# Performance work log

Measured on AMD Instinct MI355X. Metric: run time of the kernel, lower is better.

The kernel has to match this reference:

```python
import jax, jax.numpy as jnp
import numpy as np

B, S, D, UNITS = 8, 2048, 512, 512

def setup_inputs() -> dict:
    key = jax.random.key(0)
    k1, k2, k3, k4, k5 = jax.random.split(key, 5)
    inputs = jax.random.normal(k1, (B, S, D), dtype=jnp.float32)
    scale = 1.0 / np.sqrt(D)
    Ww = jax.random.normal(k2, (D, UNITS), dtype=jnp.float32) * scale
    Wb = jnp.zeros((UNITS,), dtype=jnp.float32)
    Uw = jax.random.normal(k3, (D, UNITS), dtype=jnp.float32) * scale
    Ub = jnp.zeros((UNITS,), dtype=jnp.float32)
    return {"inputs": inputs, "Ww": Ww, "Wb": Wb, "Uw": Uw, "Ub": Ub}

def reference(inputs, Ww, Wb, Uw, Ub):
    # query/key projections: [B,S,units]
    query = jnp.einsum('bsd,du->bsu', inputs, Ww) + Wb
    key_ = jnp.einsum('bsd,du->bsu', inputs, Uw) + Ub
    # unscaled scores [B,S,S], softmax over last axis
    scores = jnp.einsum('bqu,bku->bqk', query, key_)
    attn = jax.nn.softmax(scores, axis=-1)
    # context uses raw inputs as values
    context = jnp.einsum('bqk,bkd->bqd', attn, inputs)
    return context
```

## Files before the change

kernel.cpp:

```cpp
#include <hip/hip_runtime.h>
#include <stdint.h>

#define B_ 8
#define S_ 2048
#define D_ 512
#define U_ 512
#define M_TOTAL (B_*S_)
#define NPROJ (2*U_)

typedef __attribute__((ext_vector_type(8))) _Float16 f16x8;
typedef __attribute__((ext_vector_type(4))) float f32x4;

__device__ __forceinline__ uint16_t f2h(float f){
  return __builtin_bit_cast(uint16_t, (_Float16)f);
}

__device__ __forceinline__ void gload16(const void* g, void* l){
  __builtin_amdgcn_global_load_lds(
      (const __attribute__((address_space(1))) void*)g,
      (__attribute__((address_space(3))) void*)l, 16, 0, 0);
}

template<int ROWS>
__device__ __forceinline__ void stage_half(char* lbase, const uint16_t* __restrict__ gpanel,
                                           int ld, int wv, int lane){
  int r0 = wv*8 + (lane>>3);
  int gs = ((lane&7) ^ (r0&7)) << 3;
  gload16(gpanel + (size_t)r0*ld + gs, lbase + wv*1024);
  if constexpr (ROWS==128){
    gload16(gpanel + (size_t)(r0+64)*ld + gs, lbase + 8192 + wv*1024);
  }
}

__global__ __launch_bounds__(256) void prep_w(const float* __restrict__ Ww,
                                              const float* __restrict__ Uw,
                                              uint16_t* __restrict__ WT){
  int idx = blockIdx.x*256 + threadIdx.x;
  int u = idx >> 9;
  int d = idx & 511;
  float v = (u < U_) ? Ww[d*U_ + u] : Uw[d*U_ + (u-U_)];
  WT[idx] = f2h(v);
}

__global__ __launch_bounds__(256) void prep_x(const float* __restrict__ X,
                                              uint16_t* __restrict__ Xf,
                                              uint16_t* __restrict__ XT){
  __shared__ float tile[32][33];
  int b = blockIdx.z;
  int s0 = blockIdx.x * 32;
  int d0 = blockIdx.y * 32;
  int tid = threadIdx.x;
  int tr = tid >> 5;
  int tc = tid & 31;
  const float* Xb = X + (size_t)b*S_*D_;
#pragma unroll
  for (int i = 0; i < 32; i += 8){
    size_t off = (size_t)(s0+tr+i)*D_ + d0+tc;
    float v = Xb[off];
    tile[tr+i][tc] = v;
    Xf[(size_t)b*S_*D_ + off] = f2h(v);
  }
  __syncthreads();
  uint16_t* XTb = XT + (size_t)b*D_*S_;
#pragma unroll
  for (int i = 0; i < 32; i += 8)
    XTb[(size_t)(d0+tr+i)*S_ + s0+tc] = f2h(tile[tc][tr+i]);
}

#define MODE_PROJ 0
#define MODE_SCORES 1
#define MODE_PV 2

template<int MODE, int BM>
__global__ __launch_bounds__(512, 2) void gemm8p(
    const uint16_t* __restrict__ A, long long strideA, int lda,
    const uint16_t* __restrict__ Bp, long long strideB, int ldb,
    float* __restrict__ Cf, long long strideC, int ldc,
    uint16_t* __restrict__ Qo, uint16_t* __restrict__ Ko,
    const float* __restrict__ biasW, const float* __restrict__ biasU,
    int KD)
{
  constexpr int BMH   = BM/2;
  constexpr int MFR   = BMH/16;
  constexpr int AHALF = BMH*128;
  constexpr int BHALF = 128*128;
  constexpr int DSTR  = 2*AHALF + 2*BHALF;
  constexpr int ALOADS = (BMH==128) ? 2 : 1;
  __shared__ __align__(16) char smem[2*DSTR];

  const int z  = blockIdx.z;
  const int m0 = blockIdx.y * BM;
  const int n0 = blockIdx.x * 256;
  const uint16_t* Apan = A  + strideA*z + (size_t)m0*lda;
  const uint16_t* Bpan = Bp + strideB*z + (size_t)n0*ldb;

  const int t512 = threadIdx.x;
  const int wv   = t512 >> 6;
  const int lane = t512 & 63;
  const int wm   = wv >> 2;
  const int wn   = wv & 3;
  const int fr   = lane & 15;
  const int fg   = lane >> 4;
  const int sw   = fr & 7;

  const int NT = KD >> 6;

  auto Aslot = [&](int par, int h){ return smem + par*DSTR + h*AHALF; };
  auto Bslot = [&](int par, int h){ return smem + par*DSTR + 2*AHALF + h*BHALF; };

  stage_half<BMH>(Aslot(0,0), Apan,                      lda, wv, lane);
  stage_half<BMH>(Aslot(0,1), Apan + (size_t)BMH*lda,    lda, wv, lane);
  stage_half<128>(Bslot(0,0), Bpan,                      ldb, wv, lane);
  stage_half<128>(Bslot(0,1), Bpan + (size_t)128*ldb,    ldb, wv, lane);
  if (NT > 1)
    stage_half<BMH>(Aslot(1,0), Apan + 64,               lda, wv, lane);
  if constexpr (ALOADS==2) asm volatile("s_waitcnt vmcnt(2)" ::: "memory");
  else                     asm volatile("s_waitcnt vmcnt(1)" ::: "memory");
  __builtin_amdgcn_s_barrier();

  f32x4 acc[MFR][4];
#pragma unroll
  for (int i=0;i<MFR;i++)
#pragma unroll
    for (int j=0;j<4;j++) acc[i][j] = (f32x4){0.f,0.f,0.f,0.f};

  for (int t = 0; t < NT; ++t){
    const int p = t & 1;
    const char* myA = Aslot(p, wm);
    const char* myB = Bslot(p, wn>>1);
    f16x8 af[MFR];

    auto rdA = [&](int ks){
#pragma unroll
      for (int mf=0; mf<MFR; ++mf)
        af[mf] = *(const f16x8*)(myA + (mf*16+fr)*128 + (((ks<<2)|fg) ^ sw)*16);
    };
    auto rdB = [&](int ks, int nh, f16x8& b0, f16x8& b1){
      int rb = (wn&1)*64 + nh*32 + fr;
      b0 = *(const f16x8*)(myB + rb*128      + (((ks<<2)|fg) ^ sw)*16);
      b1 = *(const f16x8*)(myB + (rb+16)*128 + (((ks<<2)|fg) ^ sw)*16);
    };
    auto mm = [&](int nh, f16x8 b0, f16x8 b1){
      __builtin_amdgcn_s_setprio(1);
#pragma unroll
      for (int mf=0; mf<MFR; ++mf){
        acc[mf][nh*2]   = __builtin_amdgcn_mfma_f32_16x16x32_f16(af[mf], b0, acc[mf][nh*2],   0,0,0);
        acc[mf][nh*2+1] = __builtin_amdgcn_mfma_f32_16x16x32_f16(af[mf], b1, acc[mf][nh*2+1], 0,0,0);
      }
      __builtin_amdgcn_s_setprio(0);
    };

    f16x8 b0, b1;
    rdA(0); rdB(0, 0, b0, b1);
    if (t+1 < NT)
      stage_half<BMH>(Aslot(p^1,1), Apan + (size_t)BMH*lda + (t+1)*64, lda, wv, lane);
    __builtin_amdgcn_s_barrier();
    mm(0, b0, b1);
    __builtin_amdgcn_s_barrier();
    rdB(0, 1, b0, b1);
    if (t+1 < NT)
      stage_half<128>(Bslot(p^1,0), Bpan + (t+1)*64, ldb, wv, lane);
    __builtin_amdgcn_s_barrier();
    mm(1, b0, b1);
    __builtin_amdgcn_s_barrier();
    rdA(1); rdB(1, 0, b0, b1);
    if (t+1 < NT)
      stage_half<128>(Bslot(p^1,1), Bpan + (size_t)128*ldb + (t+1)*64, ldb, wv, lane);
    __builtin_amdgcn_s_barrier();
    mm(0, b0, b1);
    __builtin_amdgcn_s_barrier();
    rdB(1, 1, b0, b1);
    if (t+2 < NT)
      stage_half<BMH>(Aslot(p,0), Apan + (t+2)*64, lda, wv, lane);
    __builtin_amdgcn_s_barrier();
    mm(1, b0, b1);
    if constexpr (ALOADS==2) asm volatile("s_waitcnt vmcnt(2)" ::: "memory");
    else                     asm volatile("s_waitcnt vmcnt(1)" ::: "memory");
    __builtin_amdgcn_s_barrier();
  }

#pragma unroll
  for (int mf=0; mf<MFR; ++mf)
#pragma unroll
    for (int nf=0; nf<4; ++nf){
      int col  = n0 + wn*64 + nf*16 + fr;
      int rowb = m0 + wm*BMH + mf*16 + fg*4;
      f32x4 a = acc[mf][nf];
      if constexpr (MODE==MODE_PROJ){
        float bias = (col < U_) ? biasW[col] : biasU[col - U_];
        if (col < U_){
#pragma unroll
          for (int r=0;r<4;r++) Qo[(size_t)(rowb+r)*U_ + col] = f2h(a[r] + bias);
        } else {
#pragma unroll
          for (int r=0;r<4;r++) Ko[(size_t)(rowb+r)*U_ + col - U_] = f2h(a[r] + bias);
        }
      } else {
        float* C = Cf + strideC*z;
#pragma unroll
        for (int r=0;r<4;r++)
          C[(size_t)(rowb+r)*ldc + col] = a[r];
      }
    }
}

__global__ __launch_bounds__(256) void softmax_rows(float* __restrict__ SPbase)
{
  const long long row = (long long)blockIdx.y * S_ + blockIdx.x;
  float* Srow = SPbase + row * (long long)S_;
  const int t = threadIdx.x;
  const int lane = t & 63, wave = t >> 6;
  float4 x0 = *((const float4*)Srow + t*2);
  float4 x1 = *((const float4*)Srow + t*2 + 1);
  float v[8] = {x0.x,x0.y,x0.z,x0.w,x1.x,x1.y,x1.z,x1.w};
  float mx = v[0];
#pragma unroll
  for (int j=1;j<8;j++) mx = fmaxf(mx, v[j]);
#pragma unroll
  for (int off=1; off<64; off<<=1) mx = fmaxf(mx, __shfl_xor(mx, off));
  __shared__ float redm[4], reds[4];
  if (lane==0) redm[wave] = mx;
  __syncthreads();
  mx = fmaxf(fmaxf(redm[0],redm[1]), fmaxf(redm[2],redm[3]));
  float sum = 0.f;
#pragma unroll
  for (int j=0;j<8;j++){ v[j] = expf(v[j]-mx); sum += v[j]; }
#pragma unroll
  for (int off=1; off<64; off<<=1) sum += __shfl_xor(sum, off);
  if (lane==0) reds[wave] = sum;
  __syncthreads();
  sum = reds[0]+reds[1]+reds[2]+reds[3];
  float inv = 1.0f / sum;
  uint16_t o[8];
#pragma unroll
  for (int j=0;j<8;j++) o[j] = f2h(v[j]*inv);
  uint16_t* Prow = (uint16_t*)Srow;
  *((ushort4*)Prow + t*2)     = make_ushort4(o[0],o[1],o[2],o[3]);
  *((ushort4*)Prow + t*2 + 1) = make_ushort4(o[4],o[5],o[6],o[7]);
}

extern "C" void kernel_launch(void* const* d_in, const int* in_sizes, int n_in,
                              void* d_out, int out_size, void* d_ws, size_t ws_size,
                              hipStream_t stream)
{
  (void)in_sizes; (void)n_in; (void)out_size;
  const float* X  = (const float*)d_in[0];
  const float* Ww = (const float*)d_in[1];
  const float* Wb = (const float*)d_in[2];
  const float* Uw = (const float*)d_in[3];
  const float* Ub = (const float*)d_in[4];
  float* out = (float*)d_out;

  char* ws = (char*)d_ws;
  size_t off = 0;
  uint16_t* Xf = (uint16_t*)(ws + off); off += (size_t)M_TOTAL*D_*2;
  uint16_t* XT = (uint16_t*)(ws + off); off += (size_t)B_*D_*S_*2;
  uint16_t* WT = (uint16_t*)(ws + off); off += (size_t)NPROJ*D_*2;
  uint16_t* Qf = (uint16_t*)(ws + off); off += (size_t)M_TOTAL*U_*2;
  uint16_t* Kf = (uint16_t*)(ws + off); off += (size_t)M_TOTAL*U_*2;
  char* SP = ws + off;
  size_t per_b = (size_t)S_*S_*4;
  int g = 8;
  while (g > 1 && off + per_b*(size_t)g > ws_size) g >>= 1;

  prep_w<<<dim3((NPROJ*D_)/256), 256, 0, stream>>>(Ww, Uw, WT);
  prep_x<<<dim3(S_/32, D_/32, B_), 256, 0, stream>>>(X, Xf, XT);

  gemm8p<MODE_PROJ,256><<<dim3(NPROJ/256, M_TOTAL/256, 1), 512, 0, stream>>>(
      Xf, 0, D_, WT, 0, D_,
      nullptr, 0, 0, Qf, Kf, Wb, Ub, D_);

  for (int b0 = 0; b0 < B_; b0 += g) {
    gemm8p<MODE_SCORES,256><<<dim3(S_/256, S_/256, g), 512, 0, stream>>>(
        Qf + (size_t)b0*S_*U_, (long long)S_*U_, U_,
        Kf + (size_t)b0*S_*U_, (long long)S_*U_, U_,
        (float*)SP, (long long)S_*S_, S_,
        nullptr, nullptr, nullptr, nullptr, U_);
    softmax_rows<<<dim3(S_, g), 256, 0, stream>>>((float*)SP);
    gemm8p<MODE_PV,128><<<dim3(D_/256, S_/128, g), 512, 0, stream>>>(
        (const uint16_t*)SP, 2LL*S_*S_, 2*S_,
        XT + (size_t)b0*D_*S_, (long long)D_*S_, S_,
        out + (size_t)b0*S_*D_, (long long)S_*D_, D_,
        nullptr, nullptr, nullptr, nullptr, S_);
  }
}
```

Before: 163.6 us.

## Fuse scores, softmax and PV into a single flash-attention kernel

Replaces the separate scores GEMM, row softmax and PV GEMM with one flash-attention kernel that streams K and V tiles through LDS and keeps an online max and sum per query row. This removes the materialized fp32 SxS score matrix and its write and reread traffic. The kernel also skips rescaling the accumulator unless the running max grows by more than a threshold. It uses small 64x64 tiles with many barriers per iteration, and the K staging is only partly overlapped with compute, so MFMA utilization may be lower than in the tuned GEMM.

```diff
diff --git a/kernel.cpp b/kernel.cpp
--- a/kernel.cpp
+++ b/kernel.cpp
@@ -7,6 +7,9 @@
 #define U_ 512
 #define M_TOTAL (B_*S_)
 #define NPROJ (2*U_)
+#define QBLK 64
+#define KVBLK 64
+#define NIT (S_/KVBLK)
 
 typedef __attribute__((ext_vector_type(8))) _Float16 f16x8;
 typedef __attribute__((ext_vector_type(4))) float f32x4;
@@ -67,32 +70,24 @@
     XTb[(size_t)(d0+tr+i)*S_ + s0+tc] = f2h(tile[tc][tr+i]);
 }
 
-#define MODE_PROJ 0
-#define MODE_SCORES 1
-#define MODE_PV 2
-
-template<int MODE, int BM>
-__global__ __launch_bounds__(512, 2) void gemm8p(
-    const uint16_t* __restrict__ A, long long strideA, int lda,
-    const uint16_t* __restrict__ Bp, long long strideB, int ldb,
-    float* __restrict__ Cf, long long strideC, int ldc,
+__global__ __launch_bounds__(512, 2) void gemm_proj(
+    const uint16_t* __restrict__ A, int lda,
+    const uint16_t* __restrict__ Bp, int ldb,
     uint16_t* __restrict__ Qo, uint16_t* __restrict__ Ko,
     const float* __restrict__ biasW, const float* __restrict__ biasU,
     int KD)
 {
-  constexpr int BMH   = BM/2;
-  constexpr int MFR   = BMH/16;
+  constexpr int BMH   = 128;
+  constexpr int MFR   = 8;
   constexpr int AHALF = BMH*128;
   constexpr int BHALF = 128*128;
   constexpr int DSTR  = 2*AHALF + 2*BHALF;
-  constexpr int ALOADS = (BMH==128) ? 2 : 1;
   __shared__ __align__(16) char smem[2*DSTR];
 
-  const int z  = blockIdx.z;
-  const int m0 = blockIdx.y * BM;
+  const int m0 = blockIdx.y * 256;
   const int n0 = blockIdx.x * 256;
-  const uint16_t* Apan = A  + strideA*z + (size_t)m0*lda;
-  const uint16_t* Bpan = Bp + strideB*z + (size_t)n0*ldb;
+  const uint16_t* Apan = A  + (size_t)m0*lda;
+  const uint16_t* Bpan = Bp + (size_t)n0*ldb;
 
   const int t512 = threadIdx.x;
   const int wv   = t512 >> 6;
@@ -108,14 +103,13 @@
   auto Aslot = [&](int par, int h){ return smem + par*DSTR + h*AHALF; };
   auto Bslot = [&](int par, int h){ return smem + par*DSTR + 2*AHALF + h*BHALF; };
 
-  stage_half<BMH>(Aslot(0,0), Apan,                      lda, wv, lane);
-  stage_half<BMH>(Aslot(0,1), Apan + (size_t)BMH*lda,    lda, wv, lane);
-  stage_half<128>(Bslot(0,0), Bpan,                      ldb, wv, lane);
-  stage_half<128>(Bslot(0,1), Bpan + (size_t)128*ldb,    ldb, wv, lane);
+  stage_half<128>(Aslot(0,0), Apan,                   lda, wv, lane);
+  stage_half<128>(Aslot(0,1), Apan + (size_t)128*lda, lda, wv, lane);
+  stage_half<128>(Bslot(0,0), Bpan,                   ldb, wv, lane);
+  stage_half<128>(Bslot(0,1), Bpan + (size_t)128*ldb, ldb, wv, lane);
   if (NT > 1)
-    stage_half<BMH>(Aslot(1,0), Apan + 64,               lda, wv, lane);
-  if constexpr (ALOADS==2) asm volatile("s_waitcnt vmcnt(2)" ::: "memory");
-  else                     asm volatile("s_waitcnt vmcnt(1)" ::: "memory");
+    stage_half<128>(Aslot(1,0), Apan + 64,            lda, wv, lane);
+  asm volatile("s_waitcnt vmcnt(2)" ::: "memory");
   __builtin_amdgcn_s_barrier();
 
   f32x4 acc[MFR][4];
@@ -153,7 +147,7 @@
     f16x8 b0, b1;
     rdA(0); rdB(0, 0, b0, b1);
     if (t+1 < NT)
-      stage_half<BMH>(Aslot(p^1,1), Apan + (size_t)BMH*lda + (t+1)*64, lda, wv, lane);
+      stage_half<128>(Aslot(p^1,1), Apan + (size_t)128*lda + (t+1)*64, lda, wv, lane);
     __builtin_amdgcn_s_barrier();
     mm(0, b0, b1);
     __builtin_amdgcn_s_barrier();
@@ -171,11 +165,10 @@
     __builtin_amdgcn_s_barrier();
     rdB(1, 1, b0, b1);
     if (t+2 < NT)
-      stage_half<BMH>(Aslot(p,0), Apan + (t+2)*64, lda, wv, lane);
+      stage_half<128>(Aslot(p,0), Apan + (t+2)*64, lda, wv, lane);
     __builtin_amdgcn_s_barrier();
     mm(1, b0, b1);
-    if constexpr (ALOADS==2) asm volatile("s_waitcnt vmcnt(2)" ::: "memory");
-    else                     asm volatile("s_waitcnt vmcnt(1)" ::: "memory");
+    asm volatile("s_waitcnt vmcnt(2)" ::: "memory");
     __builtin_amdgcn_s_barrier();
   }
 
@@ -184,66 +177,208 @@
 #pragma unroll
     for (int nf=0; nf<4; ++nf){
       int col  = n0 + wn*64 + nf*16 + fr;
-      int rowb = m0 + wm*BMH + mf*16 + fg*4;
+      int rowb = m0 + wm*128 + mf*16 + fg*4;
       f32x4 a = acc[mf][nf];
-      if constexpr (MODE==MODE_PROJ){
-        float bias = (col < U_) ? biasW[col] : biasU[col - U_];
-        if (col < U_){
-#pragma unroll
-          for (int r=0;r<4;r++) Qo[(size_t)(rowb+r)*U_ + col] = f2h(a[r] + bias);
-        } else {
-#pragma unroll
-          for (int r=0;r<4;r++) Ko[(size_t)(rowb+r)*U_ + col - U_] = f2h(a[r] + bias);
-        }
+      float bias = (col < U_) ? biasW[col] : biasU[col - U_];
+      if (col < U_){
+#pragma unroll
+        for (int r=0;r<4;r++) Qo[(size_t)(rowb+r)*U_ + col] = f2h(a[r] + bias);
       } else {
-        float* C = Cf + strideC*z;
-#pragma unroll
-        for (int r=0;r<4;r++)
-          C[(size_t)(rowb+r)*ldc + col] = a[r];
+#pragma unroll
+        for (int r=0;r<4;r++) Ko[(size_t)(rowb+r)*U_ + col - U_] = f2h(a[r] + bias);
       }
     }
 }
 
-__global__ __launch_bounds__(256) void softmax_rows(float* __restrict__ SPbase)
+__global__ __launch_bounds__(512, 2) void flash_attn(
+    const uint16_t* __restrict__ Qf,
+    const uint16_t* __restrict__ Kf,
+    const uint16_t* __restrict__ XT,
+    float* __restrict__ Out)
 {
-  const long long row = (long long)blockIdx.y * S_ + blockIdx.x;
-  float* Srow = SPbase + row * (long long)S_;
-  const int t = threadIdx.x;
-  const int lane = t & 63, wave = t >> 6;
-  float4 x0 = *((const float4*)Srow + t*2);
-  float4 x1 = *((const float4*)Srow + t*2 + 1);
-  float v[8] = {x0.x,x0.y,x0.z,x0.w,x1.x,x1.y,x1.z,x1.w};
-  float mx = v[0];
-#pragma unroll
-  for (int j=1;j<8;j++) mx = fmaxf(mx, v[j]);
-#pragma unroll
-  for (int off=1; off<64; off<<=1) mx = fmaxf(mx, __shfl_xor(mx, off));
-  __shared__ float redm[4], reds[4];
-  if (lane==0) redm[wave] = mx;
-  __syncthreads();
-  mx = fmaxf(fmaxf(redm[0],redm[1]), fmaxf(redm[2],redm[3]));
-  float sum = 0.f;
-#pragma unroll
-  for (int j=0;j<8;j++){ v[j] = expf(v[j]-mx); sum += v[j]; }
-#pragma unroll
-  for (int off=1; off<64; off<<=1) sum += __shfl_xor(sum, off);
-  if (lane==0) reds[wave] = sum;
-  __syncthreads();
-  sum = reds[0]+reds[1]+reds[2]+reds[3];
-  float inv = 1.0f / sum;
-  uint16_t o[8];
-#pragma unroll
-  for (int j=0;j<8;j++) o[j] = f2h(v[j]*inv);
-  uint16_t* Prow = (uint16_t*)Srow;
-  *((ushort4*)Prow + t*2)     = make_ushort4(o[0],o[1],o[2],o[3]);
-  *((ushort4*)Prow + t*2 + 1) = make_ushort4(o[4],o[5],o[6],o[7]);
+  __shared__ __align__(16) uint16_t Ks[KVBLK][512];
+  __shared__ __align__(16) uint16_t Vs[512][KVBLK];
+  __shared__ __align__(16) float    Ss[QBLK][68];
+  __shared__ __align__(16) uint16_t Ps[QBLK][KVBLK];
+  __shared__ float m_s[QBLK], l_s[QBLK], f_s[QBLK];
+
+  const int bid   = blockIdx.x;
+  const int batch = bid & 7;
+  const int mblk  = bid >> 3;
+  const int s0    = mblk * QBLK;
+
+  const int t    = threadIdx.x;
+  const int wv   = t >> 6;
+  const int lane = t & 63;
+  const int fr   = lane & 15;
+  const int fg   = lane >> 4;
+  const int qg = wv >> 1;
+  const int kh = wv & 1;
+  const int wm = wv >> 2;
+  const int wd = wv & 3;
+
+  const uint16_t* Qrow = Qf + ((size_t)batch*S_ + s0)*U_;
+  const uint16_t* Krow = Kf + (size_t)batch*S_*U_;
+  const uint16_t* Vt   = XT + (size_t)batch*D_*S_;
+
+  f16x8 qreg[16];
+#pragma unroll
+  for (int kk=0; kk<16; ++kk)
+    qreg[kk] = *(const f16x8*)(Qrow + (size_t)(qg*16+fr)*U_ + kk*32 + fg*8);
+
+  auto stageK = [&](int ti){
+    const uint16_t* src = Krow + (size_t)(ti*KVBLK)*U_;
+#pragma unroll
+    for (int i=0;i<8;++i){
+      int r = i*8 + wv;
+      gload16(src + (size_t)r*U_ + ((lane ^ (r&7))<<3),
+              (char*)Ks + i*8192 + wv*1024);
+    }
+  };
+  auto stageV = [&](int ti){
+    const uint16_t* src = Vt + ti*KVBLK;
+#pragma unroll
+    for (int i=0;i<8;++i){
+      int d = i*64 + wv*8 + (lane>>3);
+      int g = lane & 7;
+      gload16(src + (size_t)d*S_ + ((g ^ (d&7))<<3),
+              (char*)Vs + i*8192 + wv*1024);
+    }
+  };
+
+  stageK(0);
+  if (t < QBLK){ m_s[t] = -3e38f; l_s[t] = 0.f; }
+  f32x4 acc[2][8];
+#pragma unroll
+  for (int i=0;i<2;i++)
+#pragma unroll
+    for (int j=0;j<8;j++) acc[i][j] = (f32x4){0.f,0.f,0.f,0.f};
+  asm volatile("s_waitcnt lgkmcnt(0)" ::: "memory");
+  __builtin_amdgcn_s_barrier();
+
+  for (int it=0; it<NIT; ++it){
+    stageV(it);
+    asm volatile("s_waitcnt vmcnt(8)" ::: "memory");
+
+    f32x4 sfr0 = (f32x4){0.f,0.f,0.f,0.f};
+    f32x4 sfr1 = (f32x4){0.f,0.f,0.f,0.f};
+    __builtin_amdgcn_s_setprio(1);
+#pragma unroll
+    for (int kk=0; kk<16; ++kk){
+      int gA = kk*4 + fg;
+      int kr0 = kh*32 + fr;
+      int kr1 = kh*32 + 16 + fr;
+      f16x8 bv0 = *(const f16x8*)((const char*)Ks + kr0*1024 + ((gA ^ (kr0&7))<<4));
+      f16x8 bv1 = *(const f16x8*)((const char*)Ks + kr1*1024 + ((gA ^ (kr1&7))<<4));
+      sfr0 = __builtin_amdgcn_mfma_f32_16x16x32_f16(qreg[kk], bv0, sfr0, 0,0,0);
+      sfr1 = __builtin_amdgcn_mfma_f32_16x16x32_f16(qreg[kk], bv1, sfr1, 0,0,0);
+    }
+    __builtin_amdgcn_s_setprio(0);
+#pragma unroll
+    for (int r=0;r<4;++r){
+      Ss[qg*16 + fg*4 + r][kh*32 + fr]      = sfr0[r];
+      Ss[qg*16 + fg*4 + r][kh*32 + 16 + fr] = sfr1[r];
+    }
+    asm volatile("s_waitcnt lgkmcnt(0)" ::: "memory");
+    __builtin_amdgcn_s_barrier();
+
+    {
+      const int r = t >> 3, j = t & 7;
+      float4 v0 = *(const float4*)&Ss[r][j*8];
+      float4 v1 = *(const float4*)&Ss[r][j*8+4];
+      float pm = fmaxf(fmaxf(fmaxf(v0.x,v0.y),fmaxf(v0.z,v0.w)),
+                       fmaxf(fmaxf(v1.x,v1.y),fmaxf(v1.z,v1.w)));
+      pm = fmaxf(pm, __shfl_xor(pm, 1));
+      pm = fmaxf(pm, __shfl_xor(pm, 2));
+      pm = fmaxf(pm, __shfl_xor(pm, 4));
+      float mo = m_s[r];
+      float mn = (pm > mo + 8.f) ? pm : mo;
+      float p0 = __expf(v0.x-mn), p1 = __expf(v0.y-mn), p2 = __expf(v0.z-mn), p3 = __expf(v0.w-mn);
+      float p4 = __expf(v1.x-mn), p5 = __expf(v1.y-mn), p6 = __expf(v1.z-mn), p7 = __expf(v1.w-mn);
+      float sum = ((p0+p1)+(p2+p3)) + ((p4+p5)+(p6+p7));
+      sum += __shfl_xor(sum, 1);
+      sum += __shfl_xor(sum, 2);
+      sum += __shfl_xor(sum, 4);
+      if (j == 0){
+        float f = __expf(mo - mn);
+        f_s[r] = f;
+        m_s[r] = mn;
+        l_s[r] = l_s[r]*f + sum;
+      }
+      f16x8 pv;
+      pv[0]=(_Float16)p0; pv[1]=(_Float16)p1; pv[2]=(_Float16)p2; pv[3]=(_Float16)p3;
+      pv[4]=(_Float16)p4; pv[5]=(_Float16)p5; pv[6]=(_Float16)p6; pv[7]=(_Float16)p7;
+      *(f16x8*)((char*)Ps + r*128 + ((j ^ (r&7))<<4)) = pv;
+    }
+    asm volatile("s_waitcnt lgkmcnt(0)" ::: "memory");
+    __builtin_amdgcn_s_barrier();
+
+    asm volatile("s_waitcnt vmcnt(0)" ::: "memory");
+    if (it+1 < NIT) stageK(it+1);
+
+    float fx[2][4];
+#pragma unroll
+    for (int mf=0; mf<2; ++mf)
+#pragma unroll
+      for (int r=0; r<4; ++r)
+        fx[mf][r] = f_s[wm*32 + mf*16 + fg*4 + r];
+    bool nr = (fx[0][0]!=1.f)|(fx[0][1]!=1.f)|(fx[0][2]!=1.f)|(fx[0][3]!=1.f)|
+              (fx[1][0]!=1.f)|(fx[1][1]!=1.f)|(fx[1][2]!=1.f)|(fx[1][3]!=1.f);
+    if (__any(nr)){
+#pragma unroll
+      for (int mf=0; mf<2; ++mf)
+#pragma unroll
+        for (int nf=0; nf<8; ++nf)
+#pragma unroll
+          for (int r=0; r<4; ++r)
+            acc[mf][nf][r] *= fx[mf][r];
+    }
+
+    __builtin_amdgcn_s_setprio(1);
+#pragma unroll
+    for (int ks=0; ks<2; ++ks){
+      int gP = ks*4 + fg;
+      int q0 = wm*32 + fr;
+      int q1 = wm*32 + 16 + fr;
+      f16x8 pa0 = *(const f16x8*)((const char*)Ps + q0*128 + ((gP ^ (q0&7))<<4));
+      f16x8 pa1 = *(const f16x8*)((const char*)Ps + q1*128 + ((gP ^ (q1&7))<<4));
+#pragma unroll
+      for (int nf=0; nf<8; ++nf){
+        int d = wd*128 + nf*16 + fr;
+        f16x8 bv = *(const f16x8*)((const char*)Vs + d*128 + ((gP ^ (d&7))<<4));
+        acc[0][nf] = __builtin_amdgcn_mfma_f32_16x16x32_f16(pa0, bv, acc[0][nf], 0,0,0);
+        acc[1][nf] = __builtin_amdgcn_mfma_f32_16x16x32_f16(pa1, bv, acc[1][nf], 0,0,0);
+      }
+    }
+    __builtin_amdgcn_s_setprio(0);
+    __builtin_amdgcn_s_barrier();
+  }
+
+  float linv[2][4];
+#pragma unroll
+  for (int mf=0; mf<2; ++mf)
+#pragma unroll
+    for (int r=0; r<4; ++r)
+      linv[mf][r] = 1.0f / l_s[wm*32 + mf*16 + fg*4 + r];
+  float* Ob = Out + ((size_t)batch*S_ + s0)*D_;
+#pragma unroll
+  for (int mf=0; mf<2; ++mf)
+#pragma unroll
+    for (int nf=0; nf<8; ++nf){
+      int d = wd*128 + nf*16 + fr;
+#pragma unroll
+      for (int r=0; r<4; ++r){
+        int q = wm*32 + mf*16 + fg*4 + r;
+        Ob[(size_t)q*D_ + d] = acc[mf][nf][r] * linv[mf][r];
+      }
+    }
 }
 
 extern "C" void kernel_launch(void* const* d_in, const int* in_sizes, int n_in,
                               void* d_out, int out_size, void* d_ws, size_t ws_size,
                               hipStream_t stream)
 {
-  (void)in_sizes; (void)n_in; (void)out_size;
+  (void)in_sizes; (void)n_in; (void)out_size; (void)ws_size;
   const float* X  = (const float*)d_in[0];
   const float* Ww = (const float*)d_in[1];
   const float* Wb = (const float*)d_in[2];
@@ -258,29 +393,12 @@
   uint16_t* WT = (uint16_t*)(ws + off); off += (size_t)NPROJ*D_*2;
   uint16_t* Qf = (uint16_t*)(ws + off); off += (size_t)M_TOTAL*U_*2;
   uint16_t* Kf = (uint16_t*)(ws + off); off += (size_t)M_TOTAL*U_*2;
-  char* SP = ws + off;
-  size_t per_b = (size_t)S_*S_*4;
-  int g = 8;
-  while (g > 1 && off + per_b*(size_t)g > ws_size) g >>= 1;
 
   prep_w<<<dim3((NPROJ*D_)/256), 256, 0, stream>>>(Ww, Uw, WT);
   prep_x<<<dim3(S_/32, D_/32, B_), 256, 0, stream>>>(X, Xf, XT);
 
-  gemm8p<MODE_PROJ,256><<<dim3(NPROJ/256, M_TOTAL/256, 1), 512, 0, stream>>>(
-      Xf, 0, D_, WT, 0, D_,
-      nullptr, 0, 0, Qf, Kf, Wb, Ub, D_);
-
-  for (int b0 = 0; b0 < B_; b0 += g) {
-    gemm8p<MODE_SCORES,256><<<dim3(S_/256, S_/256, g), 512, 0, stream>>>(
-        Qf + (size_t)b0*S_*U_, (long long)S_*U_, U_,
-        Kf + (size_t)b0*S_*U_, (long long)S_*U_, U_,
-        (float*)SP, (long long)S_*S_, S_,
-        nullptr, nullptr, nullptr, nullptr, U_);
-    softmax_rows<<<dim3(S_, g), 256, 0, stream>>>((float*)SP);
-    gemm8p<MODE_PV,128><<<dim3(D_/256, S_/128, g), 512, 0, stream>>>(
-        (const uint16_t*)SP, 2LL*S_*S_, 2*S_,
-        XT + (size_t)b0*D_*S_, (long long)D_*S_, S_,
-        out + (size_t)b0*S_*D_, (long long)S_*D_, D_,
-        nullptr, nullptr, nullptr, nullptr, S_);
-  }
-}
+  gemm_proj<<<dim3(NPROJ/256, M_TOTAL/256, 1), 512, 0, stream>>>(
+      Xf, D_, WT, D_, Qf, Kf, Wb, Ub, D_);
+
+  flash_attn<<<dim3(B_ * (S_/QBLK)), 512, 0, stream>>>(Qf, Kf, XT, out);
+}
```

New measurement: 161.2 us. Within noise of the previous version (-1.5%).
